# Optimization experiments

Measured on AMD Instinct MI355X. Metric: run time of the kernel, lower is better.

Reference implementation:

```python
import jax, jax.numpy as jnp
import numpy as np

CL1_K = 25
CL2_K = 25


def cheb_stack(L, x0, K):
    # x0: (V, M) -> (K, V, M) Chebyshev basis T_k(L) x0
    if K == 1:
        return x0[None]
    x1 = L @ x0
    if K == 2:
        return jnp.stack([x0, x1])

    def step(carry, _):
        xm1, xm2 = carry
        xk = 2.0 * (L @ xm1) - xm2
        return (xk, xm1), xk

    _, rest = jax.lax.scan(step, (x1, x0), None, length=K - 2)
    return jnp.concatenate([x0[None], x1[None], rest], axis=0)


def graph_conv(x, L, W, b, K):
    # x: (B, C, V) -> (B, Fout, V); matches torch Graph_Conv permute/view logic
    B, C, V = x.shape
    x0 = x.transpose(2, 1, 0).reshape(V, C * B)
    xs = cheb_stack(L, x0, K)                              # (K, V, C*B)
    xs = xs.reshape(K, V, C, B).transpose(3, 1, 2, 0)      # (B, V, C, K)
    xs = xs.reshape(B * V, C * K)
    y = xs @ W.T + b                                       # (B*V, Fout)
    return y.reshape(B, V, -1).transpose(0, 2, 1)


def maxpool4(x):
    B, C, V = x.shape
    return x.reshape(B, C, V // 4, 4).max(axis=-1)


def setup_inputs() -> dict:
    key = jax.random.key(0)
    ks = jax.random.split(key, 10)
    B, C, V, Vp = 32, 16, 4000, 4096
    CL1_F, CL2_F, FC_F = 64, 128, 10
    x = jax.random.normal(ks[0], (B, C, V), dtype=jnp.float32)
    perm = jax.random.permutation(ks[1], Vp)
    # rescaled Laplacians, scaled for stable 25-step recurrence
    L1 = jax.random.normal(ks[2], (Vp, Vp), dtype=jnp.float32) * (0.3 / np.sqrt(Vp))
    L2 = jax.random.normal(ks[3], (Vp // 4, Vp // 4), dtype=jnp.float32) * (0.3 / np.sqrt(Vp // 4))
    W1 = jax.random.normal(ks[4], (CL1_F, C * CL1_K), dtype=jnp.float32) * np.sqrt(2.0 / (C * CL1_K + CL1_F))
    b1 = jnp.zeros((CL1_F,), dtype=jnp.float32)
    W2 = jax.random.normal(ks[5], (CL2_F, CL1_F * CL2_K), dtype=jnp.float32) * np.sqrt(2.0 / (CL1_F * CL2_K + CL2_F))
    b2 = jnp.zeros((CL2_F,), dtype=jnp.float32)
    FC_IN = CL2_F * Vp // 16
    Wfc = jax.random.normal(ks[6], (FC_F, FC_IN), dtype=jnp.float32) * np.sqrt(2.0 / (FC_IN + FC_F))
    bfc = jnp.zeros((FC_F,), dtype=jnp.float32)
    return {"x": x, "perm": perm, "L1": L1, "L2": L2, "W1": W1, "b1": b1,
            "W2": W2, "b2": b2, "Wfc": Wfc, "bfc": bfc}


def reference(x, perm, L1, L2, W1, b1, W2, b2, Wfc, bfc):
    # BatchNorm1d(affine=False), training-mode batch statistics
    mu = x.mean(axis=(0, 2), keepdims=True)
    var = x.var(axis=(0, 2), keepdims=True)
    x = (x - mu) / jnp.sqrt(var + 1e-5)
    # Permute: zero-pad vertices to len(perm), then index
    B, C, V = x.shape
    Vp = perm.shape[0]
    x = jnp.pad(x, ((0, 0), (0, 0), (0, Vp - V)))[:, :, perm]
    x = jax.nn.relu(graph_conv(x, L1, W1, b1, CL1_K))
    x = maxpool4(x)
    x = jax.nn.relu(graph_conv(x, L2, W2, b2, CL2_K))
    x = maxpool4(x)
    x = x.reshape(B, -1)
    # dropout in eval mode (identity)
    return x @ Wfc.T + bfc
```

## Files before the change

kernel.cpp:

```cpp
#include <hip/hip_runtime.h>

typedef _Float16 half8 __attribute__((ext_vector_type(8)));
typedef _Float16 half4 __attribute__((ext_vector_type(4)));
typedef float f32x4 __attribute__((ext_vector_type(4)));

__device__ __forceinline__ void gload_lds16(const void* g, void* l) {
  __builtin_amdgcn_global_load_lds((const __attribute__((address_space(1))) void*)g,
                                   (__attribute__((address_space(3))) void*)l, 16, 0, 0);
}

__global__ __launch_bounds__(256) void k_bn_partial(const float* __restrict__ x,
                                                    float* __restrict__ part) {
  const int c = blockIdx.x & 15;
  const int seg = blockIdx.x >> 4;
  const int t = threadIdx.x;
  float s = 0.f, s2 = 0.f;
  for (int b = 0; b < 32; ++b) {
    const float* row = x + (size_t)(b * 16 + c) * 4000 + seg * 500;
    for (int v = t; v < 500; v += 256) {
      float val = row[v];
      s += val;
      s2 += val * val;
    }
  }
#pragma unroll
  for (int off = 32; off > 0; off >>= 1) {
    s += __shfl_down(s, off);
    s2 += __shfl_down(s2, off);
  }
  __shared__ float rs_[4], rs2_[4];
  if ((t & 63) == 0) { rs_[t >> 6] = s; rs2_[t >> 6] = s2; }
  __syncthreads();
  if (t == 0) {
    part[c * 8 + seg] = rs_[0] + rs_[1] + rs_[2] + rs_[3];
    part[128 + c * 8 + seg] = rs2_[0] + rs2_[1] + rs2_[2] + rs2_[3];
  }
}

__global__ void k_bn_final(const float* __restrict__ part, float* __restrict__ musig) {
  const int c = threadIdx.x;
  if (c < 16) {
    float S = 0.f, S2 = 0.f;
#pragma unroll
    for (int seg = 0; seg < 8; ++seg) {
      S += part[c * 8 + seg];
      S2 += part[128 + c * 8 + seg];
    }
    const float inv = 1.f / 128000.f;
    float mu = S * inv;
    float var = S2 * inv - mu * mu;
    musig[c] = mu;
    musig[16 + c] = rsqrtf(var + 1e-5f);
  }
}

__global__ __launch_bounds__(256) void k_build_x0(const float* __restrict__ x,
                                                  const int* __restrict__ perm,
                                                  const float* __restrict__ musig,
                                                  _Float16* __restrict__ X0) {
  const int idx = blockIdx.x * 256 + threadIdx.x;
  const int v = idx & 4095;
  const int m = idx >> 12;
  const int b = m & 31;
  const int c = m >> 5;
  const int pv = perm[v];
  float val = 0.f;
  if (pv < 4000)
    val = (x[((size_t)(b * 16 + c)) * 4000 + pv] - musig[c]) * musig[16 + c] * 0.0625f;
  X0[idx] = (_Float16)val;
}

__global__ __launch_bounds__(256) void k_cvt_f16(const float* __restrict__ s,
                                                 _Float16* __restrict__ d, int n) {
  const int i = (blockIdx.x * 256 + threadIdx.x) * 4;
  if (i >= n) return;
  f32x4 v = *(const f32x4*)(s + i);
  half4 h;
  h[0] = (_Float16)v[0]; h[1] = (_Float16)v[1];
  h[2] = (_Float16)v[2]; h[3] = (_Float16)v[3];
  *(half4*)(d + i) = h;
}

__global__ __launch_bounds__(256) void k_zero(_Float16* __restrict__ p, int n8) {
  const int i = blockIdx.x * 256 + threadIdx.x;
  if (i < n8) *(half8*)(p + (size_t)i * 8) = half8{};
}

__global__ __launch_bounds__(256) void k_prep_w(const float* __restrict__ W,
                                                _Float16* __restrict__ Wp,
                                                int F, int shiftC, int kround) {
  const int idx = blockIdx.x * 256 + threadIdx.x;
  const int CS = 1 << shiftC;
  const int KPtot = kround * CS;
  if (idx >= F * KPtot) return;
  const int f = idx / KPtot;
  const int rem = idx - f * KPtot;
  const int k = rem >> shiftC;
  const int c = rem & (CS - 1);
  float v = 0.f;
  if (k < 25) v = W[(size_t)f * (CS * 25) + c * 25 + k];
  Wp[idx] = (_Float16)v;
}

__global__ __launch_bounds__(512, 1) void k_cheb_ks(const _Float16* __restrict__ Xprev,
                                                    const _Float16* __restrict__ Lm,
                                                    _Float16* __restrict__ P) {
  __shared__ _Float16 lds[2][32768];
  const int t = threadIdx.x;
  const int lane = t & 63;
  const int g = lane >> 4;
  const int w = t >> 6;
  const int wm = w >> 2, wn = w & 3;
  const int bid = blockIdx.x;
  const int bx = bid & 15;
  const int kq = (bid >> 4) & 7;
  const int by = bid >> 7;
  const int v0 = bx * 256, m0 = by * 256;
  const size_t rs = 8192;

  const char* Ag = (const char*)Xprev + (size_t)m0 * rs + (size_t)kq * 1024;
  const char* Bg = (const char*)Lm + (size_t)v0 * rs + (size_t)kq * 1024;

  f32x4 acc[8][4] = {};

  auto stage = [&](int buf, int tt) {
    char* A = (char*)&lds[buf][0];
    char* B = (char*)&lds[buf][16384];
#pragma unroll
    for (int j = 0; j < 4; ++j) {
      const int ch = j * 512 + t;
      const int row = ch >> 3, c8 = ch & 7;
      gload_lds16(Ag + (size_t)row * rs + tt * 128 + ((c8 ^ (row & 7)) << 4), A + ch * 16);
    }
#pragma unroll
    for (int j = 0; j < 4; ++j) {
      const int ch = j * 512 + t;
      const int row = ch >> 3, c8 = ch & 7;
      gload_lds16(Bg + (size_t)row * rs + tt * 128 + ((c8 ^ (row & 7)) << 4), B + ch * 16);
    }
  };

  stage(0, 0);

  for (int tt = 0; tt < 8; ++tt) {
    const int cur = tt & 1;
    if (tt + 1 < 8) {
      stage(cur ^ 1, tt + 1);
      asm volatile("s_waitcnt vmcnt(8)" ::: "memory");
    } else {
      asm volatile("s_waitcnt vmcnt(0)" ::: "memory");
    }
    asm volatile("s_barrier" ::: "memory");
    const char* A = (const char*)&lds[cur][0];
    const char* B = (const char*)&lds[cur][16384];
#pragma unroll
    for (int kk = 0; kk < 2; ++kk) {
      const int cb = kk * 64 + (g << 4);
      half8 a[8], b[4];
#pragma unroll
      for (int mi = 0; mi < 8; ++mi) {
        const int ar = wm * 128 + mi * 16 + (lane & 15);
        a[mi] = *(const half8*)(A + ar * 128 + (cb ^ ((ar & 7) << 4)));
      }
#pragma unroll
      for (int ni = 0; ni < 4; ++ni) {
        const int br = wn * 64 + ni * 16 + (lane & 15);
        b[ni] = *(const half8*)(B + br * 128 + (cb ^ ((br & 7) << 4)));
      }
#pragma unroll
      for (int mi = 0; mi < 8; ++mi)
#pragma unroll
        for (int ni = 0; ni < 4; ++ni)
          acc[mi][ni] = __builtin_amdgcn_mfma_f32_16x16x32_f16(a[mi], b[ni], acc[mi][ni], 0, 0, 0);
    }
    asm volatile("s_barrier" ::: "memory");
  }

  _Float16* Pq = P + (size_t)kq * 2097152;
  const int rb = g << 2;
#pragma unroll
  for (int mi = 0; mi < 8; ++mi) {
#pragma unroll
    for (int ni = 0; ni < 4; ++ni) {
      const int vv = v0 + wn * 64 + ni * 16 + (lane & 15);
#pragma unroll
      for (int r = 0; r < 4; ++r) {
        const int mm = m0 + wm * 128 + mi * 16 + rb + r;
        Pq[(size_t)mm * 4096 + vv] = (_Float16)acc[mi][ni][r];
      }
    }
  }
}

__global__ __launch_bounds__(256) void k_cheb_red(const _Float16* __restrict__ P,
                                                  const _Float16* __restrict__ Xm2,
                                                  _Float16* __restrict__ Xout,
                                                  float alpha, float beta) {
  const size_t i = ((size_t)blockIdx.x * 256 + threadIdx.x) * 8;
  float s[8] = {};
#pragma unroll
  for (int p = 0; p < 8; ++p) {
    half8 v = *(const half8*)(P + (size_t)p * 2097152 + i);
#pragma unroll
    for (int j = 0; j < 8; ++j) s[j] += (float)v[j];
  }
  half8 xm2 = {};
  if (beta != 0.f) xm2 = *(const half8*)(Xm2 + i);
  half8 o;
#pragma unroll
  for (int j = 0; j < 8; ++j) o[j] = (_Float16)(alpha * s[j] - beta * (float)xm2[j]);
  *(half8*)(Xout + i) = o;
}

__global__ __launch_bounds__(512, 2) void k_cheb(const _Float16* __restrict__ Xprev,
                                                 const _Float16* __restrict__ Lm,
                                                 const _Float16* __restrict__ Xm2,
                                                 _Float16* __restrict__ Xout,
                                                 int V, float alpha, float beta) {
  __shared__ _Float16 lds[2][2][12288];
  const int t = threadIdx.x;
  const int lane = t & 63;
  const int w = t >> 6;
  const int kh = w >> 2;
  const int wl = w & 3;
  const int wr = wl >> 1, wc = wl & 1;
  const int v0 = blockIdx.x * 64;
  const int m0 = blockIdx.y * 128;
  const size_t rs = (size_t)V * 2;
  const int K2 = V >> 1;
  const int NT2 = K2 >> 6;

  const char* Ag = (const char*)Xprev + (size_t)m0 * rs + (size_t)kh * K2 * 2;
  const char* Bg = (const char*)Lm + (size_t)v0 * rs + (size_t)kh * K2 * 2;
  const size_t soff = (size_t)(lane >> 3) * rs + (size_t)(((lane & 7) * 16) ^ ((lane >> 3) << 4));

  f32x4 acc[4][2] = {};

  auto stage = [&](int buf, int tt) {
    const char* ag = Ag + (size_t)tt * 128 + soff;
    const char* bg = Bg + (size_t)tt * 128 + soff;
    char* A = (char*)&lds[kh][buf][0];
    char* B = (char*)&lds[kh][buf][8192];
#pragma unroll
    for (int j = 0; j < 4; ++j) {
      const int r0 = wl * 32 + j * 8;
      gload_lds16(ag + (size_t)r0 * rs, A + r0 * 128);
    }
#pragma unroll
    for (int j = 0; j < 2; ++j) {
      const int r0 = wl * 16 + j * 8;
      gload_lds16(bg + (size_t)r0 * rs, B + r0 * 128);
    }
  };

  stage(0, 0);

  for (int tt = 0; tt < NT2; ++tt) {
    const int cur = tt & 1;
    if (tt + 1 < NT2) {
      stage(cur ^ 1, tt + 1);
      asm volatile("s_waitcnt vmcnt(6)" ::: "memory");
    } else {
      asm volatile("s_waitcnt vmcnt(0)" ::: "memory");
    }
    asm volatile("s_barrier" ::: "memory");
    const char* A = (const char*)&lds[kh][cur][0];
    const char* B = (const char*)&lds[kh][cur][8192];
#pragma unroll
    for (int kk = 0; kk < 2; ++kk) {
      const int cb = kk * 64 + ((lane >> 4) << 4);
      half8 a[4], b[2];
#pragma unroll
      for (int mi = 0; mi < 4; ++mi) {
        const int ar = wr * 64 + mi * 16 + (lane & 15);
        a[mi] = *(const half8*)(A + ar * 128 + (cb ^ ((ar & 7) << 4)));
      }
#pragma unroll
      for (int ni = 0; ni < 2; ++ni) {
        const int br = wc * 32 + ni * 16 + (lane & 15);
        b[ni] = *(const half8*)(B + br * 128 + (cb ^ ((br & 7) << 4)));
      }
#pragma unroll
      for (int mi = 0; mi < 4; ++mi)
#pragma unroll
        for (int ni = 0; ni < 2; ++ni)
          acc[mi][ni] = __builtin_amdgcn_mfma_f32_16x16x32_f16(a[mi], b[ni], acc[mi][ni], 0, 0, 0);
    }
    asm volatile("s_barrier" ::: "memory");
  }

  __syncthreads();
  float* red = (float*)&lds[0][0][0];
  if (kh == 1) {
    float* dst = red + wl * 2048 + lane * 4;
#pragma unroll
    for (int mi = 0; mi < 4; ++mi)
#pragma unroll
      for (int ni = 0; ni < 2; ++ni)
        *(f32x4*)(dst + (mi * 2 + ni) * 256) = acc[mi][ni];
  }
  __syncthreads();
  if (kh == 0) {
    const float* src = red + wl * 2048 + lane * 4;
    const int rbase = (lane >> 4) << 2;
#pragma unroll
    for (int mi = 0; mi < 4; ++mi) {
#pragma unroll
      for (int ni = 0; ni < 2; ++ni) {
        f32x4 o = *(const f32x4*)(src + (mi * 2 + ni) * 256);
        const int vv = v0 + wc * 32 + ni * 16 + (lane & 15);
#pragma unroll
        for (int r = 0; r < 4; ++r) {
          const int mm = m0 + wr * 64 + mi * 16 + rbase + r;
          const size_t idx = (size_t)mm * V + vv;
          float val = alpha * (acc[mi][ni][r] + o[r]);
          if (beta != 0.f) val -= (float)Xm2[idx];
          Xout[idx] = (_Float16)val;
        }
      }
    }
  }
}

template <int FT>
__global__ __launch_bounds__(256, 2) void k_dense(const _Float16* __restrict__ Wp,
                                                  const _Float16* __restrict__ XS,
                                                  const float* __restrict__ bias,
                                                  float* __restrict__ Yt,
                                                  int Vv, int shiftC, int nsteps,
                                                  int Ntot, float ascale, float bscale) {
  __shared__ _Float16 Alds[2][FT * 64];
  __shared__ _Float16 Blds[2][64 * 64];
  const int t = threadIdx.x;
  const int lane = t & 63;
  const int g = lane >> 4;
  const int w = t >> 6;
  const int n0 = blockIdx.x * 64;
  const int b = n0 / Vv;
  const int vb = n0 % Vv;
  const int Kp = nsteps * 64;
  const int cmask = (1 << shiftC) - 1;
  const size_t plane = 2097152;

  f32x4 acc[FT / 16] = {};

  auto stage = [&](int buf, int s) {
    const int q0 = s * 64;
    char* A = (char*)&Alds[buf][0];
    char* B = (char*)&Blds[buf][0];
#pragma unroll
    for (int j = 0; j < FT / 32; ++j) {
      const int ch = j * 256 + t;
      const int f = ch >> 3, c8 = ch & 7;
      gload_lds16((const char*)Wp + ((size_t)f * Kp + q0) * 2 + ((c8 ^ (f & 7)) << 4),
                  A + ch * 16);
    }
#pragma unroll
    for (int j = 0; j < 2; ++j) {
      const int ch = j * 256 + t;
      const int q = ch >> 3, c8 = ch & 7;
      const int qq = q0 + q;
      const int k = qq >> shiftC, c = qq & cmask;
      const int sz = (q >> 3) & 7;
      gload_lds16((const char*)XS + ((size_t)k * plane + (size_t)(c * 32 + b) * Vv + vb) * 2 +
                      ((c8 ^ sz) << 4),
                  B + ch * 16);
    }
  };

  stage(0, 0);

  for (int s = 0; s < nsteps; ++s) {
    const int cur = s & 1;
    if (s + 1 < nsteps) {
      stage(cur ^ 1, s + 1);
      if constexpr (FT == 64) {
        asm volatile("s_waitcnt vmcnt(4)" ::: "memory");
      } else {
        asm volatile("s_waitcnt vmcnt(6)" ::: "memory");
      }
    } else {
      asm volatile("s_waitcnt vmcnt(0)" ::: "memory");
    }
    asm volatile("s_barrier" ::: "memory");
    const _Float16* A = &Alds[cur][0];
    const _Float16* B = &Blds[cur][0];
#pragma unroll
    for (int kk = 0; kk < 2; ++kk) {
      half8 bf;
      const int c = lane & 15;
#pragma unroll
      for (int j = 0; j < 8; ++j) {
        const int q = kk * 32 + g * 8 + j;
        const int sz = (q >> 3) & 7;
        bf[j] = B[q * 64 + ((w * 16 + c) ^ (sz << 3))];
      }
#pragma unroll
      for (int mi = 0; mi < FT / 16; ++mi) {
        const int ar = mi * 16 + c;
        half8 af = *(const half8*)((const char*)A + ar * 128 +
                                   ((kk * 64 + g * 16) ^ ((ar & 7) << 4)));
        acc[mi] = __builtin_amdgcn_mfma_f32_16x16x32_f16(af, bf, acc[mi], 0, 0, 0);
      }
    }
    asm volatile("s_barrier" ::: "memory");
  }

  const int n = n0 + w * 16 + (lane & 15);
#pragma unroll
  for (int mi = 0; mi < FT / 16; ++mi) {
#pragma unroll
    for (int r = 0; r < 4; ++r) {
      const int f = mi * 16 + g * 4 + r;
      Yt[(size_t)f * Ntot + n] = fmaxf(ascale * acc[mi][r] + bscale * bias[f], 0.f);
    }
  }
}

__global__ __launch_bounds__(256) void k_pool1(const float* __restrict__ Yt,
                                               _Float16* __restrict__ X2) {
  const int idx = blockIdx.x * 256 + threadIdx.x;
  const int v2 = idx & 1023;
  const int rest = idx >> 10;
  const int b = rest & 31;
  const int f = rest >> 5;
  f32x4 q = *(const f32x4*)(Yt + (size_t)f * 131072 + b * 4096 + v2 * 4);
  float mx = fmaxf(fmaxf(q[0], q[1]), fmaxf(q[2], q[3]));
  X2[(size_t)(f * 32 + b) * 1024 + v2] = (_Float16)(mx * 0.015625f);
}

__global__ __launch_bounds__(256) void k_pool2(const float* __restrict__ Yt,
                                               float* __restrict__ p2) {
  const int idx = blockIdx.x * 256 + threadIdx.x;
  const int v3 = idx & 255;
  const int rest = idx >> 8;
  const int f = rest & 127;
  const int b = rest >> 7;
  f32x4 q = *(const f32x4*)(Yt + (size_t)f * 32768 + b * 1024 + v3 * 4);
  float mx = fmaxf(fmaxf(q[0], q[1]), fmaxf(q[2], q[3]));
  p2[(size_t)b * 32768 + f * 256 + v3] = mx;
}

__global__ __launch_bounds__(256) void k_fc_part(const float* __restrict__ p2,
                                                 const float* __restrict__ Wfc,
                                                 float* __restrict__ partF) {
  const int b = blockIdx.x >> 3;
  const int seg = blockIdx.x & 7;
  const int t = threadIdx.x;
  const int lane = t & 63;
  const int w = t >> 6;
  const int base = seg * 4096;
  float acc[10];
#pragma unroll
  for (int o = 0; o < 10; ++o) acc[o] = 0.f;
  const float* pb = p2 + (size_t)b * 32768 + base;
  for (int i = t; i < 4096; i += 256) {
    float p = pb[i];
#pragma unroll
    for (int o = 0; o < 10; ++o) acc[o] += p * Wfc[(size_t)o * 32768 + base + i];
  }
#pragma unroll
  for (int off = 32; off > 0; off >>= 1)
#pragma unroll
    for (int o = 0; o < 10; ++o) acc[o] += __shfl_down(acc[o], off);
  __shared__ float rws[10][4];
  if (lane == 0) {
#pragma unroll
    for (int o = 0; o < 10; ++o) rws[o][w] = acc[o];
  }
  __syncthreads();
  if (t < 10) partF[blockIdx.x * 10 + t] =
      rws[t][0] + rws[t][1] + rws[t][2] + rws[t][3];
}

__global__ void k_fc_final(const float* __restrict__ partF,
                           const float* __restrict__ bfc,
                           float* __restrict__ out) {
  const int t = threadIdx.x;
  if (t < 320) {
    const int b = t / 10, o = t - b * 10;
    float s = 0.f;
#pragma unroll
    for (int seg = 0; seg < 8; ++seg) s += partF[(b * 8 + seg) * 10 + o];
    out[b * 10 + o] = 64.f * s + bfc[o];
  }
}

extern "C" void kernel_launch(void* const* d_in, const int* in_sizes, int n_in,
                              void* d_out, int out_size, void* d_ws, size_t ws_size,
                              hipStream_t stream) {
  (void)in_sizes; (void)n_in; (void)out_size; (void)ws_size;
  const float* x = (const float*)d_in[0];
  const int* perm = (const int*)d_in[1];
  const float* L1 = (const float*)d_in[2];
  const float* L2 = (const float*)d_in[3];
  const float* W1 = (const float*)d_in[4];
  const float* b1 = (const float*)d_in[5];
  const float* W2 = (const float*)d_in[6];
  const float* b2 = (const float*)d_in[7];
  const float* Wfc = (const float*)d_in[8];
  const float* bfc = (const float*)d_in[9];
  float* out = (float*)d_out;

  char* ws = (char*)d_ws;
  size_t off = 0;
  auto alloc = [&](size_t bytes) {
    char* p = ws + off;
    off += (bytes + 255) & ~(size_t)255;
    return p;
  };
  _Float16* L1h = (_Float16*)alloc(16777216ull * 2);
  _Float16* L2h = (_Float16*)alloc(1048576ull * 2);
  _Float16* W1p = (_Float16*)alloc(64ull * 448 * 2);
  _Float16* W2p = (_Float16*)alloc(128ull * 1664 * 2);
  float* part = (float*)alloc(256 * 4);
  float* musig = (float*)alloc(32 * 4);
  float* partF = (float*)alloc(2560 * 4);
  _Float16* XS = (_Float16*)alloc(28ull * 2097152 * 2);
  float* Yt = (float*)alloc(64ull * 131072 * 4);
  float* p2 = (float*)alloc(32ull * 128 * 256 * 4);
  _Float16* Pq = (_Float16*)Yt;

  const size_t plane = 2097152;

  k_cvt_f16<<<16384, 256, 0, stream>>>(L1, L1h, 16777216);
  k_cvt_f16<<<1024, 256, 0, stream>>>(L2, L2h, 1048576);
  k_prep_w<<<112, 256, 0, stream>>>(W1, W1p, 64, 4, 28);
  k_prep_w<<<832, 256, 0, stream>>>(W2, W2p, 128, 6, 26);
  k_zero<<<3072, 256, 0, stream>>>(XS + 25 * plane, 786432);
  k_bn_partial<<<128, 256, 0, stream>>>(x, part);
  k_bn_final<<<1, 64, 0, stream>>>(part, musig);
  k_build_x0<<<8192, 256, 0, stream>>>(x, perm, musig, XS);

  for (int k = 1; k < 25; ++k) {
    k_cheb_ks<<<256, 512, 0, stream>>>(XS + (size_t)(k - 1) * plane, L1h, Pq);
    k_cheb_red<<<1024, 256, 0, stream>>>(
        Pq, XS + (size_t)(k >= 2 ? k - 2 : 0) * plane, XS + (size_t)k * plane,
        (k == 1) ? 1.f : 2.f, (k == 1) ? 0.f : 1.f);
  }
  k_dense<64><<<dim3(2048, 1), 256, 0, stream>>>(W1p, XS, b1, Yt, 4096, 4, 7,
                                                 131072, 16.f, 1.f);
  k_pool1<<<8192, 256, 0, stream>>>(Yt, XS);
  for (int k = 1; k < 25; ++k) {
    k_cheb<<<dim3(16, 16), 512, 0, stream>>>(
        XS + (size_t)(k - 1) * plane, L2h,
        XS + (size_t)(k >= 2 ? k - 2 : 0) * plane, XS + (size_t)k * plane,
        1024, (k == 1) ? 1.f : 2.f, (k == 1) ? 0.f : 1.f);
  }
  k_dense<128><<<dim3(512, 1), 256, 0, stream>>>(W2p, XS, b2, Yt, 1024, 6, 26,
                                                 32768, 1.f, 0.015625f);
  k_pool2<<<4096, 256, 0, stream>>>(Yt, p2);
  k_fc_part<<<256, 256, 0, stream>>>(p2, Wfc, partF);
  k_fc_final<<<1, 320, 0, stream>>>(partF, bfc, out);
}
```

Measured before the change: 1.283 ms.

## Unify Chebyshev GEMMs into split-K kernel with triple-buffered LDS pipeline

Replaces both Chebyshev recurrence GEMM kernels with one parameterized split-K kernel. It uses 128x256 tiles, four K splits, a three-stage LDS ring with half-tile prefetch interleaved into the MFMA loop, and setprio around the MFMA block. The layer-2 recurrence now also uses split-K plus a separate reduction kernel instead of the in-block two-way K reduction. The intent is higher occupancy (two blocks per CU) and better overlap of loads with compute. The cost is more partial-sum traffic and an extra launch per step for layer 2.

```diff
diff --git a/kernel.cpp b/kernel.cpp
--- a/kernel.cpp
+++ b/kernel.cpp
@@ -102,104 +102,116 @@
   Wp[idx] = (_Float16)v;
 }
 
-__global__ __launch_bounds__(512, 1) void k_cheb_ks(const _Float16* __restrict__ Xprev,
-                                                    const _Float16* __restrict__ Lm,
-                                                    _Float16* __restrict__ P) {
-  __shared__ _Float16 lds[2][32768];
+__global__ __launch_bounds__(512, 2) void k_cheb8(const _Float16* __restrict__ Xprev,
+                                                  const _Float16* __restrict__ Lm,
+                                                  _Float16* __restrict__ P,
+                                                  int V, int NT, int bxbits, int bybits) {
+  __shared__ _Float16 lds[3][24576];
   const int t = threadIdx.x;
   const int lane = t & 63;
+  const int ln = lane & 15;
   const int g = lane >> 4;
+  const int g16 = g << 4;
   const int w = t >> 6;
   const int wm = w >> 2, wn = w & 3;
   const int bid = blockIdx.x;
-  const int bx = bid & 15;
-  const int kq = (bid >> 4) & 7;
-  const int by = bid >> 7;
-  const int v0 = bx * 256, m0 = by * 256;
-  const size_t rs = 8192;
-
-  const char* Ag = (const char*)Xprev + (size_t)m0 * rs + (size_t)kq * 1024;
-  const char* Bg = (const char*)Lm + (size_t)v0 * rs + (size_t)kq * 1024;
-
-  f32x4 acc[8][4] = {};
-
-  auto stage = [&](int buf, int tt) {
-    char* A = (char*)&lds[buf][0];
-    char* B = (char*)&lds[buf][16384];
-#pragma unroll
-    for (int j = 0; j < 4; ++j) {
-      const int ch = j * 512 + t;
-      const int row = ch >> 3, c8 = ch & 7;
-      gload_lds16(Ag + (size_t)row * rs + tt * 128 + ((c8 ^ (row & 7)) << 4), A + ch * 16);
-    }
-#pragma unroll
-    for (int j = 0; j < 4; ++j) {
-      const int ch = j * 512 + t;
-      const int row = ch >> 3, c8 = ch & 7;
-      gload_lds16(Bg + (size_t)row * rs + tt * 128 + ((c8 ^ (row & 7)) << 4), B + ch * 16);
+  const int bx = bid & ((1 << bxbits) - 1);
+  const int by = (bid >> bxbits) & ((1 << bybits) - 1);
+  const int kq = bid >> (bxbits + bybits);
+  const int v0 = bx * 256, m0 = by * 128;
+  const size_t rs = (size_t)V * 2;
+  const int koffB = kq * NT * 128;
+
+  const char* Ag = (const char*)Xprev + (size_t)m0 * rs + koffB;
+  const char* Bg = (const char*)Lm + (size_t)v0 * rs + koffB;
+
+  f32x4 acc[4][4] = {};
+
+  auto stageHalf = [&](int buf, int tt, int half) {
+    char* Lb = (char*)&lds[buf][0];
+#pragma unroll
+    for (int j = 0; j < 3; ++j) {
+      const int idx = half * 1536 + j * 512 + t;
+      if (idx < 1024) {
+        const int row = idx >> 3, c8 = idx & 7;
+        gload_lds16(Ag + (size_t)row * rs + tt * 128 + ((c8 ^ (row & 7)) << 4),
+                    Lb + idx * 16);
+      } else {
+        const int bi = idx - 1024;
+        const int row = bi >> 3, c8 = bi & 7;
+        gload_lds16(Bg + (size_t)row * rs + tt * 128 + ((c8 ^ (row & 7)) << 4),
+                    Lb + 16384 + bi * 16);
+      }
     }
   };
 
-  stage(0, 0);
-
-  for (int tt = 0; tt < 8; ++tt) {
-    const int cur = tt & 1;
-    if (tt + 1 < 8) {
-      stage(cur ^ 1, tt + 1);
-      asm volatile("s_waitcnt vmcnt(8)" ::: "memory");
-    } else {
-      asm volatile("s_waitcnt vmcnt(0)" ::: "memory");
-    }
-    asm volatile("s_barrier" ::: "memory");
+  stageHalf(0, 0, 0); stageHalf(0, 0, 1);
+  stageHalf(1, 1, 0); stageHalf(1, 1, 1);
+  asm volatile("s_waitcnt vmcnt(6)" ::: "memory");
+  asm volatile("s_barrier" ::: "memory");
+
+  for (int tt = 0; tt < NT; ++tt) {
+    const int cur = tt % 3;
+    const int nxt = (tt + 2) % 3;
     const char* A = (const char*)&lds[cur][0];
-    const char* B = (const char*)&lds[cur][16384];
+    const char* B = A + 16384;
 #pragma unroll
     for (int kk = 0; kk < 2; ++kk) {
-      const int cb = kk * 64 + (g << 4);
-      half8 a[8], b[4];
-#pragma unroll
-      for (int mi = 0; mi < 8; ++mi) {
-        const int ar = wm * 128 + mi * 16 + (lane & 15);
-        a[mi] = *(const half8*)(A + ar * 128 + (cb ^ ((ar & 7) << 4)));
+      half8 a[4], b[4];
+#pragma unroll
+      for (int mi = 0; mi < 4; ++mi) {
+        const int ar = wm * 64 + mi * 16 + ln;
+        a[mi] = *(const half8*)(A + ar * 128 + ((kk * 64 + g16) ^ ((ar & 7) << 4)));
       }
 #pragma unroll
       for (int ni = 0; ni < 4; ++ni) {
-        const int br = wn * 64 + ni * 16 + (lane & 15);
-        b[ni] = *(const half8*)(B + br * 128 + (cb ^ ((br & 7) << 4)));
-      }
-#pragma unroll
-      for (int mi = 0; mi < 8; ++mi)
+        const int br = wn * 64 + ni * 16 + ln;
+        b[ni] = *(const half8*)(B + br * 128 + ((kk * 64 + g16) ^ ((br & 7) << 4)));
+      }
+      if (tt + 2 < NT) stageHalf(nxt, tt + 2, kk);
+      if (kk == 1) {
+        if (tt + 2 < NT) {
+          asm volatile("s_waitcnt vmcnt(6)" ::: "memory");
+        } else {
+          asm volatile("s_waitcnt vmcnt(0)" ::: "memory");
+        }
+      }
+      asm volatile("s_barrier" ::: "memory");
+      asm volatile("s_waitcnt lgkmcnt(0)" ::: "memory");
+      __builtin_amdgcn_sched_barrier(0);
+      __builtin_amdgcn_s_setprio(1);
+#pragma unroll
+      for (int mi = 0; mi < 4; ++mi)
 #pragma unroll
         for (int ni = 0; ni < 4; ++ni)
           acc[mi][ni] = __builtin_amdgcn_mfma_f32_16x16x32_f16(a[mi], b[ni], acc[mi][ni], 0, 0, 0);
-    }
-    asm volatile("s_barrier" ::: "memory");
+      __builtin_amdgcn_s_setprio(0);
+      asm volatile("s_barrier" ::: "memory");
+    }
   }
 
   _Float16* Pq = P + (size_t)kq * 2097152;
-  const int rb = g << 2;
-#pragma unroll
-  for (int mi = 0; mi < 8; ++mi) {
+#pragma unroll
+  for (int mi = 0; mi < 4; ++mi) {
 #pragma unroll
     for (int ni = 0; ni < 4; ++ni) {
-      const int vv = v0 + wn * 64 + ni * 16 + (lane & 15);
-#pragma unroll
-      for (int r = 0; r < 4; ++r) {
-        const int mm = m0 + wm * 128 + mi * 16 + rb + r;
-        Pq[(size_t)mm * 4096 + vv] = (_Float16)acc[mi][ni][r];
-      }
-    }
-  }
-}
-
-__global__ __launch_bounds__(256) void k_cheb_red(const _Float16* __restrict__ P,
-                                                  const _Float16* __restrict__ Xm2,
-                                                  _Float16* __restrict__ Xout,
-                                                  float alpha, float beta) {
+      const int vv = v0 + wn * 64 + ni * 16 + ln;
+      const int mmb = m0 + wm * 64 + mi * 16 + g * 4;
+#pragma unroll
+      for (int r = 0; r < 4; ++r)
+        Pq[(size_t)(mmb + r) * V + vv] = (_Float16)acc[mi][ni][r];
+    }
+  }
+}
+
+__global__ __launch_bounds__(256) void k_cheb_red4(const _Float16* __restrict__ P,
+                                                   const _Float16* __restrict__ Xm2,
+                                                   _Float16* __restrict__ Xout,
+                                                   float alpha, float beta) {
   const size_t i = ((size_t)blockIdx.x * 256 + threadIdx.x) * 8;
   float s[8] = {};
 #pragma unroll
-  for (int p = 0; p < 8; ++p) {
+  for (int p = 0; p < 4; ++p) {
     half8 v = *(const half8*)(P + (size_t)p * 2097152 + i);
 #pragma unroll
     for (int j = 0; j < 8; ++j) s[j] += (float)v[j];
@@ -210,116 +222,6 @@
 #pragma unroll
   for (int j = 0; j < 8; ++j) o[j] = (_Float16)(alpha * s[j] - beta * (float)xm2[j]);
   *(half8*)(Xout + i) = o;
-}
-
-__global__ __launch_bounds__(512, 2) void k_cheb(const _Float16* __restrict__ Xprev,
-                                                 const _Float16* __restrict__ Lm,
-                                                 const _Float16* __restrict__ Xm2,
-                                                 _Float16* __restrict__ Xout,
-                                                 int V, float alpha, float beta) {
-  __shared__ _Float16 lds[2][2][12288];
-  const int t = threadIdx.x;
-  const int lane = t & 63;
-  const int w = t >> 6;
-  const int kh = w >> 2;
-  const int wl = w & 3;
-  const int wr = wl >> 1, wc = wl & 1;
-  const int v0 = blockIdx.x * 64;
-  const int m0 = blockIdx.y * 128;
-  const size_t rs = (size_t)V * 2;
-  const int K2 = V >> 1;
-  const int NT2 = K2 >> 6;
-
-  const char* Ag = (const char*)Xprev + (size_t)m0 * rs + (size_t)kh * K2 * 2;
-  const char* Bg = (const char*)Lm + (size_t)v0 * rs + (size_t)kh * K2 * 2;
-  const size_t soff = (size_t)(lane >> 3) * rs + (size_t)(((lane & 7) * 16) ^ ((lane >> 3) << 4));
-
-  f32x4 acc[4][2] = {};
-
-  auto stage = [&](int buf, int tt) {
-    const char* ag = Ag + (size_t)tt * 128 + soff;
-    const char* bg = Bg + (size_t)tt * 128 + soff;
-    char* A = (char*)&lds[kh][buf][0];
-    char* B = (char*)&lds[kh][buf][8192];
-#pragma unroll
-    for (int j = 0; j < 4; ++j) {
-      const int r0 = wl * 32 + j * 8;
-      gload_lds16(ag + (size_t)r0 * rs, A + r0 * 128);
-    }
-#pragma unroll
-    for (int j = 0; j < 2; ++j) {
-      const int r0 = wl * 16 + j * 8;
-      gload_lds16(bg + (size_t)r0 * rs, B + r0 * 128);
-    }
-  };
-
-  stage(0, 0);
-
-  for (int tt = 0; tt < NT2; ++tt) {
-    const int cur = tt & 1;
-    if (tt + 1 < NT2) {
-      stage(cur ^ 1, tt + 1);
-      asm volatile("s_waitcnt vmcnt(6)" ::: "memory");
-    } else {
-      asm volatile("s_waitcnt vmcnt(0)" ::: "memory");
-    }
-    asm volatile("s_barrier" ::: "memory");
-    const char* A = (const char*)&lds[kh][cur][0];
-    const char* B = (const char*)&lds[kh][cur][8192];
-#pragma unroll
-    for (int kk = 0; kk < 2; ++kk) {
-      const int cb = kk * 64 + ((lane >> 4) << 4);
-      half8 a[4], b[2];
-#pragma unroll
-      for (int mi = 0; mi < 4; ++mi) {
-        const int ar = wr * 64 + mi * 16 + (lane & 15);
-        a[mi] = *(const half8*)(A + ar * 128 + (cb ^ ((ar & 7) << 4)));
-      }
-#pragma unroll
-      for (int ni = 0; ni < 2; ++ni) {
-        const int br = wc * 32 + ni * 16 + (lane & 15);
-        b[ni] = *(const half8*)(B + br * 128 + (cb ^ ((br & 7) << 4)));
-      }
-#pragma unroll
-      for (int mi = 0; mi < 4; ++mi)
-#pragma unroll
-        for (int ni = 0; ni < 2; ++ni)
-          acc[mi][ni] = __builtin_amdgcn_mfma_f32_16x16x32_f16(a[mi], b[ni], acc[mi][ni], 0, 0, 0);
-    }
-    asm volatile("s_barrier" ::: "memory");
-  }
-
-  __syncthreads();
-  float* red = (float*)&lds[0][0][0];
-  if (kh == 1) {
-    float* dst = red + wl * 2048 + lane * 4;
-#pragma unroll
-    for (int mi = 0; mi < 4; ++mi)
-#pragma unroll
-      for (int ni = 0; ni < 2; ++ni)
-        *(f32x4*)(dst + (mi * 2 + ni) * 256) = acc[mi][ni];
-  }
-  __syncthreads();
-  if (kh == 0) {
-    const float* src = red + wl * 2048 + lane * 4;
-    const int rbase = (lane >> 4) << 2;
-#pragma unroll
-    for (int mi = 0; mi < 4; ++mi) {
-#pragma unroll
-      for (int ni = 0; ni < 2; ++ni) {
-        f32x4 o = *(const f32x4*)(src + (mi * 2 + ni) * 256);
-        const int vv = v0 + wc * 32 + ni * 16 + (lane & 15);
-#pragma unroll
-        for (int r = 0; r < 4; ++r) {
-          const int mm = m0 + wr * 64 + mi * 16 + rbase + r;
-          const size_t idx = (size_t)mm * V + vv;
-          float val = alpha * (acc[mi][ni][r] + o[r]);
-          if (beta != 0.f) val -= (float)Xm2[idx];
-          Xout[idx] = (_Float16)val;
-        }
-      }
-    }
-  }
 }
 
 template <int FT>
@@ -533,8 +435,8 @@
   k_build_x0<<<8192, 256, 0, stream>>>(x, perm, musig, XS);
 
   for (int k = 1; k < 25; ++k) {
-    k_cheb_ks<<<256, 512, 0, stream>>>(XS + (size_t)(k - 1) * plane, L1h, Pq);
-    k_cheb_red<<<1024, 256, 0, stream>>>(
+    k_cheb8<<<256, 512, 0, stream>>>(XS + (size_t)(k - 1) * plane, L1h, Pq, 4096, 16, 4, 2);
+    k_cheb_red4<<<1024, 256, 0, stream>>>(
         Pq, XS + (size_t)(k >= 2 ? k - 2 : 0) * plane, XS + (size_t)k * plane,
         (k == 1) ? 1.f : 2.f, (k == 1) ? 0.f : 1.f);
   }
@@ -542,10 +444,10 @@
                                                  131072, 16.f, 1.f);
   k_pool1<<<8192, 256, 0, stream>>>(Yt, XS);
   for (int k = 1; k < 25; ++k) {
-    k_cheb<<<dim3(16, 16), 512, 0, stream>>>(
-        XS + (size_t)(k - 1) * plane, L2h,
-        XS + (size_t)(k >= 2 ? k - 2 : 0) * plane, XS + (size_t)k * plane,
-        1024, (k == 1) ? 1.f : 2.f, (k == 1) ? 0.f : 1.f);
+    k_cheb8<<<256, 512, 0, stream>>>(XS + (size_t)(k - 1) * plane, L2h, Pq, 1024, 4, 2, 4);
+    k_cheb_red4<<<1024, 256, 0, stream>>>(
+        Pq, XS + (size_t)(k >= 2 ? k - 2 : 0) * plane, XS + (size_t)k * plane,
+        (k == 1) ? 1.f : 2.f, (k == 1) ? 0.f : 1.f);
   }
   k_dense<128><<<dim3(512, 1), 256, 0, stream>>>(W2p, XS, b2, Yt, 1024, 6, 26,
                                                  32768, 1.f, 0.015625f);
```

New measurement: 1.248 ms. 1.03x faster.
